# Kernel optimization log

Hardware: AMD Instinct MI355X
Metric: run time of the kernel (lower is better)

## Reference

```python
import jax, jax.numpy as jnp
import numpy as np
import math

NUM_EXPERTS = 8
CAP_FACTOR = 1.25
MIN_CAPACITY = 4

def _capacity(num_tokens, num_experts):
    cap = math.floor(CAP_FACTOR * num_tokens / num_experts)
    cap += cap % 2
    return max(cap, MIN_CAPACITY)

def setup_inputs() -> dict:
    key = jax.random.key(0)
    k1, k2, k3, k4 = jax.random.split(key, 4)
    tokens, d_model, d_ff, E = 8192, 1024, 4096, NUM_EXPERTS
    x = jax.random.normal(k1, (tokens, d_model), dtype=jnp.float32)
    gate_weight = jax.random.normal(k2, (E, d_model), dtype=jnp.float32) * math.sqrt(0.1 / d_model)
    expert_weight = jax.random.normal(k3, (E, d_model, d_ff), dtype=jnp.float32) * 0.02
    expert_bias = jax.random.normal(k4, (E, 1, d_ff), dtype=jnp.float32) * 0.02
    return {"x": x, "gate_weight": gate_weight, "expert_weight": expert_weight, "expert_bias": expert_bias}

def reference(x, gate_weight, expert_weight, expert_bias):
    tokens, d_model = x.shape
    E = gate_weight.shape[0]
    capacity = _capacity(tokens, E)
    # FP32 gate (Switch-style)
    gate_logits = jnp.dot(x.astype(jnp.float32), gate_weight.astype(jnp.float32).T)  # [s, E]
    logits = jax.nn.softmax(gate_logits, axis=-1)  # auto_cast_softmax in fp32
    # Top-1 routing, select_policy='first'
    top1_idx = jnp.argmax(gate_logits, axis=-1)  # argmax over raw gate output
    mask = jax.nn.one_hot(top1_idx, E, dtype=jnp.int32)  # [s, E]
    # aux load-balancing loss (training path)
    me = jnp.mean(logits, axis=0)
    ce = jnp.mean(mask.astype(jnp.float32), axis=0)
    l_aux = E * jnp.sum(me * ce)
    # cumsum-based capacity ranking
    ranks = jnp.cumsum(mask, axis=0) - 1  # [s, E]
    mask = mask * (ranks < capacity).astype(jnp.int32)
    ranks_tok = jnp.sum(mask * ranks, axis=-1)  # [s]
    rank_oh = jax.nn.one_hot(ranks_tok, capacity, dtype=logits.dtype)  # [s, c]
    weight = mask.astype(logits.dtype) * logits  # [s, E]
    combine_weights = weight[:, :, None] * rank_oh[:, None, :]  # [s, E, c]
    sec_mask = combine_weights != 0  # bool dispatch mask
    # scatter dispatch: [s,E,c] x [s,d] -> [E,c,d]
    dispatched = jnp.einsum("sec,sd->ecd", sec_mask.astype(x.dtype), x)
    # per-expert front linear: [E,c,d] x [E,d,f] -> [E,c,f]
    out = jnp.einsum("ecd,edf->ecf", dispatched, expert_weight) + expert_bias
    return out, combine_weights, l_aux
```

## Files before the change

kernel.cpp:

```cpp
#include <hip/hip_runtime.h>
#include <hip/hip_bf16.h>

#define TOKENS 8192
#define DM 1024
#define DFF 4096
#define NE 8
#define CAP 1280
#define ECAP (NE*CAP)
#define OUT_ELEMS ((size_t)NE*CAP*DFF)
#define CMB_ELEMS ((size_t)TOKENS*NE*CAP)
#define ZROW TOKENS
#define GBK 32

typedef __attribute__((ext_vector_type(8))) short short8;
typedef __attribute__((ext_vector_type(16))) float f32x16;
typedef __attribute__((ext_vector_type(4))) float f4;

__device__ inline ushort f2bf(float f) {
    __hip_bfloat16 h = __float2bfloat16(f);
    return *reinterpret_cast<ushort*>(&h);
}

__device__ __forceinline__ void gload16(const ushort* g, short* l) {
    __builtin_amdgcn_global_load_lds(
        (const __attribute__((address_space(1))) void*)g,
        (__attribute__((address_space(3))) void*)l, 16, 0, 0);
}

__global__ __launch_bounds__(256) void gate_kernel(const float* __restrict__ x,
        const float* __restrict__ gw, float* __restrict__ probs8, int* __restrict__ top1,
        ushort* __restrict__ xbf) {
    int wave = threadIdx.x >> 6;
    int lane = threadIdx.x & 63;
    int t = blockIdx.x * 4 + wave;
    const float* xrow = x + (size_t)t * DM;
    float4 xv[4];
    #pragma unroll
    for (int j = 0; j < 4; ++j) xv[j] = *(const float4*)(xrow + lane * 4 + j * 256);
    ushort* xbrow = xbf + (size_t)t * DM;
    #pragma unroll
    for (int j = 0; j < 4; ++j) {
        ushort4 o;
        o.x = f2bf(xv[j].x); o.y = f2bf(xv[j].y); o.z = f2bf(xv[j].z); o.w = f2bf(xv[j].w);
        *(ushort4*)(xbrow + lane * 4 + j * 256) = o;
    }
    float logit[8];
    #pragma unroll
    for (int e = 0; e < 8; ++e) {
        const float* g = gw + e * DM;
        float s = 0.f;
        #pragma unroll
        for (int j = 0; j < 4; ++j) {
            float4 gv = *(const float4*)(g + lane * 4 + j * 256);
            s += xv[j].x * gv.x + xv[j].y * gv.y + xv[j].z * gv.z + xv[j].w * gv.w;
        }
        #pragma unroll
        for (int off = 32; off >= 1; off >>= 1) s += __shfl_xor(s, off);
        logit[e] = s;
    }
    if (lane == 0) {
        int bi = 0; float bv = logit[0];
        #pragma unroll
        for (int e = 1; e < 8; ++e) if (logit[e] > bv) { bv = logit[e]; bi = e; }
        float se = 0.f, p[8];
        #pragma unroll
        for (int e = 0; e < 8; ++e) { p[e] = expf(logit[e] - bv); se += p[e]; }
        float inv = 1.f / se;
        #pragma unroll
        for (int e = 0; e < 8; ++e) probs8[t * 8 + e] = p[e] * inv;
        top1[t] = bi;
    }
    if (blockIdx.x == 0) {
        ushort4 z; z.x = z.y = z.z = z.w = 0;
        *(ushort4*)(xbf + (size_t)ZROW * DM + threadIdx.x * 4) = z;
    }
}

__global__ __launch_bounds__(512) void cvtw_rank_kernel(
        const float* __restrict__ w, ushort* __restrict__ wt,
        const int* __restrict__ top1, const float* __restrict__ probs8,
        int* __restrict__ slot_token, int* __restrict__ pos,
        int* __restrict__ cnts, float* __restrict__ laux_out) {
    __shared__ __align__(16) char smem[TOKENS * 4 + 64 * 4 + 8 * 4];
    const int tid = threadIdx.x;
    if (blockIdx.x == 0) {
        int* t1s = (int*)smem;
        float* red = (float*)(smem + TOKENS * 4);
        int* cnt_sh = (int*)(smem + TOKENS * 4 + 64 * 4);
        int w8 = tid >> 6;
        int lane = tid & 63;
        for (int i = tid; i < TOKENS; i += 512) t1s[i] = top1[i];
        for (int i = tid; i < ECAP; i += 512) slot_token[i] = ZROW;
        for (int i = tid; i < TOKENS; i += 512) pos[i] = -1;

        float ps[8];
        #pragma unroll
        for (int e = 0; e < 8; ++e) ps[e] = 0.f;
        for (int t = tid; t < TOKENS; t += 512) {
            float4 a = *(const float4*)(probs8 + t * 8);
            float4 b = *(const float4*)(probs8 + t * 8 + 4);
            ps[0] += a.x; ps[1] += a.y; ps[2] += a.z; ps[3] += a.w;
            ps[4] += b.x; ps[5] += b.y; ps[6] += b.z; ps[7] += b.w;
        }
        #pragma unroll
        for (int e = 0; e < 8; ++e) {
            #pragma unroll
            for (int off = 32; off >= 1; off >>= 1) ps[e] += __shfl_xor(ps[e], off);
        }
        if (lane == 0) {
            #pragma unroll
            for (int e = 0; e < 8; ++e) red[w8 * 8 + e] = ps[e];
        }
        __syncthreads();

        int base = 0;
        for (int t0 = 0; t0 < TOKENS; t0 += 256) {
            #pragma unroll
            for (int q = 0; q < 4; ++q) {
                int t = t0 + q * 64 + lane;
                bool mine = (t1s[t] == w8);
                unsigned long long m = __ballot(mine);
                if (mine) {
                    int r = base + __popcll(m & ((1ull << lane) - 1ull));
                    if (r < CAP) { slot_token[w8 * CAP + r] = t; pos[t] = w8 * CAP + r; }
                }
                base += __popcll(m);
            }
        }
        if (lane == 0) { cnt_sh[w8] = base; cnts[w8] = (base < CAP) ? base : CAP; }
        __syncthreads();
        if (tid == 0) {
            float la = 0.f;
            #pragma unroll
            for (int e = 0; e < 8; ++e) {
                float me = 0.f;
                #pragma unroll
                for (int wv = 0; wv < 8; ++wv) me += red[wv * 8 + e];
                la += (me / (float)TOKENS) * ((float)cnt_sh[e] / (float)TOKENS);
            }
            laux_out[0] = la * (float)NE;
        }
        return;
    }
    float (*tile)[65] = (float(*)[65])smem;
    int b = blockIdx.x - 1;
    int e = b >> 11;
    int rem = b & 2047;
    int n0 = (rem & 63) * 64;
    int k0 = (rem >> 6) * 32;
    const float* we = w + (size_t)e * DM * DFF;
    int c = tid & 63, r0 = tid >> 6;
    #pragma unroll
    for (int i = 0; i < 4; ++i) {
        int r = r0 + i * 8;
        tile[r][c] = we[(size_t)(k0 + r) * DFF + n0 + c];
    }
    __syncthreads();
    ushort* wte = wt + (size_t)e * DFF * DM;
    int kc = tid & 31, nr0 = tid >> 5;
    #pragma unroll
    for (int i = 0; i < 4; ++i) {
        int nr = nr0 + i * 16;
        wte[(size_t)(n0 + nr) * DM + k0 + kc] = f2bf(tile[kc][nr]);
    }
}

__global__ __launch_bounds__(256, 3) void gemm_kernel(
    const ushort* __restrict__ xbf,
    const ushort* __restrict__ wt,
    const float*  __restrict__ bias,
    const int*    __restrict__ slot_token,
    const int*    __restrict__ cnts,
    float* __restrict__ out,
    const int*    __restrict__ pos,
    const float*  __restrict__ probs8,
    float* __restrict__ cmb,
    int do_combine)
{
    const int bid = blockIdx.x;
    const int e   = bid & 7;
    const int rem = bid >> 3;
    const int nt  = rem & 31;
    const int mt  = rem >> 5;
    __shared__ __align__(16) short lds[2][8192];
    const int tid  = threadIdx.x;
    const int lane = tid & 63;
    const int wave = tid >> 6;
    const int wr = wave >> 1;
    const int wc = wave & 1;
    const int ln31 = lane & 31, lh = lane >> 5;
    const int tbeg = bid * 4;
    const bool has_cmb = do_combine && (bid < 2048);

    float* orow = out + ((size_t)(e * CAP + mt * 128)) * DFF + (size_t)nt * 128;

    if (mt * 128 >= cnts[e]) {
        int c4 = tid & 31;
        int r0b = tid >> 5;
        f4 bv4 = *(const f4*)(bias + e * DFF + nt * 128 + c4 * 4);
        for (int r = r0b; r < 128; r += 8)
            __builtin_nontemporal_store(bv4, (f4*)(orow + (size_t)r * DFF + c4 * 4));
    } else {
        const int r0 = tid >> 2;
        const int kg = (tid & 3) ^ ((tid >> 3) & 3);
        const int tokA0 = slot_token[e * CAP + mt * 128 + r0];
        const int tokA1 = slot_token[e * CAP + mt * 128 + 64 + r0];
        const ushort* aptr0 = xbf + (size_t)tokA0 * DM + kg * 8;
        const ushort* aptr1 = xbf + (size_t)tokA1 * DM + kg * 8;
        const ushort* bptr0 = wt + ((size_t)e * DFF + (size_t)nt * 128 + r0) * DM + kg * 8;
        const ushort* bptr1 = bptr0 + (size_t)64 * DM;

        #define STAGE(T) do { \
            short* base_ = &lds[(T) & 1][0]; \
            size_t ko_ = (size_t)(T) * GBK; \
            gload16(aptr0 + ko_, base_ + tid * 8); \
            gload16(aptr1 + ko_, base_ + 2048 + tid * 8); \
            gload16(bptr0 + ko_, base_ + 4096 + tid * 8); \
            gload16(bptr1 + ko_, base_ + 6144 + tid * 8); \
        } while (0)

        int aoff[4], boff[4];
        #pragma unroll
        for (int s = 0; s < 2; ++s) {
            #pragma unroll
            for (int mi = 0; mi < 2; ++mi) {
                int r = wr * 64 + mi * 32 + ln31;
                int c = lh + 2 * s;
                aoff[s * 2 + mi] = (r * 4 + (c ^ ((r >> 1) & 3))) * 8;
            }
            #pragma unroll
            for (int ni = 0; ni < 2; ++ni) {
                int rn = wc * 64 + ni * 32 + ln31;
                int c = lh + 2 * s;
                boff[s * 2 + ni] = 4096 + (rn * 4 + (c ^ ((rn >> 1) & 3))) * 8;
            }
        }

        f32x16 acc[2][2];
        #pragma unroll
        for (int mi = 0; mi < 2; ++mi)
            #pragma unroll
            for (int ni = 0; ni < 2; ++ni)
                acc[mi][ni] = (f32x16)(0.f);

        STAGE(0);
        for (int t = 0; t < 32; ++t) {
            if (t < 31) {
                STAGE(t + 1);
                asm volatile("s_waitcnt vmcnt(4)" ::: "memory");
            } else {
                asm volatile("s_waitcnt vmcnt(0)" ::: "memory");
            }
            __builtin_amdgcn_s_barrier();
            __builtin_amdgcn_sched_barrier(0);

            const short* L = &lds[t & 1][0];
            __builtin_amdgcn_s_setprio(1);
            #pragma unroll
            for (int s = 0; s < 2; ++s) {
                short8 af[2], bfr[2];
                #pragma unroll
                for (int ni = 0; ni < 2; ++ni) bfr[ni] = *(const short8*)(L + boff[s * 2 + ni]);
                #pragma unroll
                for (int mi = 0; mi < 2; ++mi) af[mi] = *(const short8*)(L + aoff[s * 2 + mi]);
                #pragma unroll
                for (int mi = 0; mi < 2; ++mi)
                    #pragma unroll
                    for (int ni = 0; ni < 2; ++ni)
                        acc[mi][ni] = __builtin_amdgcn_mfma_f32_32x32x16_bf16(af[mi], bfr[ni], acc[mi][ni], 0, 0, 0);
            }
            __builtin_amdgcn_s_setprio(0);
            __builtin_amdgcn_sched_barrier(0);
            asm volatile("" ::: "memory");
            __builtin_amdgcn_s_barrier();
            asm volatile("" ::: "memory");
        }
        #undef STAGE

        #pragma unroll
        for (int ni = 0; ni < 2; ++ni) {
            int c = wc * 64 + ni * 32 + ln31;
            float bv = bias[e * DFF + nt * 128 + c];
            #pragma unroll
            for (int mi = 0; mi < 2; ++mi) {
                #pragma unroll
                for (int reg = 0; reg < 16; ++reg) {
                    int r = wr * 64 + mi * 32 + (reg & 3) + 8 * (reg >> 2) + 4 * lh;
                    __builtin_nontemporal_store(acc[mi][ni][reg] + bv,
                        orow + (size_t)r * DFF + c);
                }
            }
        }
    }

    if (has_cmb) {
        for (int i = 0; i < 4; ++i) {
            int tok = tbeg + i;
            int p = pos[tok];
            int ee = (p < 0) ? 0 : (p / CAP);
            float val = probs8[tok * 8 + ee];
            f4* row = (f4*)(cmb + (size_t)tok * ECAP);
            #pragma unroll
            for (int k = 0; k < 10; ++k) {
                int b4 = (tid + k * 256) * 4;
                f4 v;
                v.x = (b4 + 0 == p) ? val : 0.f;
                v.y = (b4 + 1 == p) ? val : 0.f;
                v.z = (b4 + 2 == p) ? val : 0.f;
                v.w = (b4 + 3 == p) ? val : 0.f;
                __builtin_nontemporal_store(v, row + tid + k * 256);
            }
        }
    }
}

__global__ __launch_bounds__(256) void combine_kernel(const int* __restrict__ pos,
        const float* __restrict__ probs8, float* __restrict__ cmb) {
    int tok = blockIdx.x;
    int p = pos[tok];
    int e = p / CAP;
    float val = probs8[tok * 8 + (e < 0 ? 0 : e)];
    f4* row = (f4*)(cmb + (size_t)tok * ECAP);
    #pragma unroll
    for (int k = 0; k < 10; ++k) {
        int c = threadIdx.x + k * 256;
        int b4 = c * 4;
        f4 v;
        v.x = (b4 + 0 == p) ? val : 0.f;
        v.y = (b4 + 1 == p) ? val : 0.f;
        v.z = (b4 + 2 == p) ? val : 0.f;
        v.w = (b4 + 3 == p) ? val : 0.f;
        __builtin_nontemporal_store(v, row + c);
    }
}

extern "C" void kernel_launch(void* const* d_in, const int* in_sizes, int n_in,
                              void* d_out, int out_size, void* d_ws, size_t ws_size,
                              hipStream_t stream) {
    const float* x  = (const float*)d_in[0];
    const float* gw = (const float*)d_in[1];
    const float* ew = (const float*)d_in[2];
    const float* eb = (const float*)d_in[3];

    float* out = (float*)d_out;
    float* cmb = out + OUT_ELEMS;
    float* laux_out = cmb + CMB_ELEMS;

    float* probs8 = (float*)d_ws;
    int* top1 = (int*)(probs8 + TOKENS * 8);
    int* slot_token = top1 + TOKENS;
    int* pos = slot_token + ECAP;
    int* cnts = pos + TOKENS;

    const size_t SMALL = 1 << 20;
    const size_t WT_ELEMS_ = (size_t)NE * DFF * DM;
    const size_t XBF_ELEMS_ = (size_t)(TOKENS + 1) * DM;
    bool big_ws = ws_size >= SMALL + (WT_ELEMS_ + XBF_ELEMS_) * sizeof(ushort);
    ushort* wtbf = big_ws ? (ushort*)((char*)d_ws + SMALL) : (ushort*)cmb;
    ushort* xbf  = wtbf + WT_ELEMS_;

    gate_kernel<<<TOKENS / 4, 256, 0, stream>>>(x, gw, probs8, top1, xbf);
    cvtw_rank_kernel<<<16385, 512, 0, stream>>>(ew, wtbf, top1, probs8,
                                                slot_token, pos, cnts, laux_out);
    if (big_ws) {
        gemm_kernel<<<2560, 256, 0, stream>>>(xbf, wtbf, eb, slot_token, cnts, out,
                                              pos, probs8, cmb, 1);
    } else {
        gemm_kernel<<<2560, 256, 0, stream>>>(xbf, wtbf, eb, slot_token, cnts, out,
                                              pos, probs8, cmb, 0);
        combine_kernel<<<TOKENS, 256, 0, stream>>>(pos, probs8, cmb);
    }
}
```

Before: 202.7 us.

## Enlarge GEMM tile to 256 rows, triple-buffer LDS, move combine zeroing to convert kernel

The expert GEMM now uses 512-thread blocks computing 256x128 tiles, which halves the grid and the reloads of weight tiles. It prefetches two k-steps ahead through a three-stage LDS ring. The dense zero-fill of the combine-weights tensor moves into extra blocks of the weight-convert/rank kernel. The GEMM then only scatters the single nonzero value per token after its tile. The aims are better operand reuse, more latency hiding, and taking the large combine store stream off the GEMM's critical path. The cost is much more LDS per block, which lowers the number of resident blocks, plus a longer convert kernel.

```diff
diff --git a/kernel.cpp b/kernel.cpp
--- a/kernel.cpp
+++ b/kernel.cpp
@@ -11,6 +11,8 @@
 #define CMB_ELEMS ((size_t)TOKENS*NE*CAP)
 #define ZROW TOKENS
 #define GBK 32
+#define NCVT 16384
+#define NZERO 4096
 
 typedef __attribute__((ext_vector_type(8))) short short8;
 typedef __attribute__((ext_vector_type(16))) float f32x16;
@@ -80,7 +82,8 @@
         const float* __restrict__ w, ushort* __restrict__ wt,
         const int* __restrict__ top1, const float* __restrict__ probs8,
         int* __restrict__ slot_token, int* __restrict__ pos,
-        int* __restrict__ cnts, float* __restrict__ laux_out) {
+        int* __restrict__ cnts, float* __restrict__ laux_out,
+        float* __restrict__ cmb, int do_zero) {
     __shared__ __align__(16) char smem[TOKENS * 4 + 64 * 4 + 8 * 4];
     const int tid = threadIdx.x;
     if (blockIdx.x == 0) {
@@ -142,6 +145,16 @@
         }
         return;
     }
+    if (blockIdx.x > NCVT) {
+        if (!do_zero) return;
+        int zb = blockIdx.x - (NCVT + 1);
+        f4 z4; z4.x = z4.y = z4.z = z4.w = 0.f;
+        f4* row = (f4*)(cmb + (size_t)zb * 2 * ECAP);
+        #pragma unroll
+        for (int k = 0; k < 10; ++k)
+            __builtin_nontemporal_store(z4, row + tid + k * 512);
+        return;
+    }
     float (*tile)[65] = (float(*)[65])smem;
     int b = blockIdx.x - 1;
     int e = b >> 11;
@@ -165,7 +178,7 @@
     }
 }
 
-__global__ __launch_bounds__(256, 3) void gemm_kernel(
+__global__ __launch_bounds__(512, 4) void gemm_kernel(
     const ushort* __restrict__ xbf,
     const ushort* __restrict__ wt,
     const float*  __restrict__ bias,
@@ -175,143 +188,135 @@
     const int*    __restrict__ pos,
     const float*  __restrict__ probs8,
     float* __restrict__ cmb,
-    int do_combine)
+    int do_scatter)
 {
     const int bid = blockIdx.x;
     const int e   = bid & 7;
     const int rem = bid >> 3;
     const int nt  = rem & 31;
     const int mt  = rem >> 5;
-    __shared__ __align__(16) short lds[2][8192];
+    __shared__ __align__(16) short lds[3][12288];
     const int tid  = threadIdx.x;
     const int lane = tid & 63;
     const int wave = tid >> 6;
     const int wr = wave >> 1;
     const int wc = wave & 1;
     const int ln31 = lane & 31, lh = lane >> 5;
-    const int tbeg = bid * 4;
-    const bool has_cmb = do_combine && (bid < 2048);
-
-    float* orow = out + ((size_t)(e * CAP + mt * 128)) * DFF + (size_t)nt * 128;
-
-    if (mt * 128 >= cnts[e]) {
+
+    float* orow = out + ((size_t)(e * CAP + mt * 256)) * DFF + (size_t)nt * 128;
+
+    #define SCATTER() do { if (do_scatter && bid < 1024 && tid < 8) { \
+        int tok_ = bid * 8 + tid; \
+        int p_ = pos[tok_]; \
+        if (p_ >= 0) cmb[(size_t)tok_ * ECAP + p_] = probs8[tok_ * 8 + p_ / CAP]; \
+    } } while (0)
+
+    if (mt * 256 >= cnts[e]) {
         int c4 = tid & 31;
         int r0b = tid >> 5;
         f4 bv4 = *(const f4*)(bias + e * DFF + nt * 128 + c4 * 4);
-        for (int r = r0b; r < 128; r += 8)
+        for (int r = r0b; r < 256; r += 16)
             __builtin_nontemporal_store(bv4, (f4*)(orow + (size_t)r * DFF + c4 * 4));
-    } else {
-        const int r0 = tid >> 2;
-        const int kg = (tid & 3) ^ ((tid >> 3) & 3);
-        const int tokA0 = slot_token[e * CAP + mt * 128 + r0];
-        const int tokA1 = slot_token[e * CAP + mt * 128 + 64 + r0];
-        const ushort* aptr0 = xbf + (size_t)tokA0 * DM + kg * 8;
-        const ushort* aptr1 = xbf + (size_t)tokA1 * DM + kg * 8;
-        const ushort* bptr0 = wt + ((size_t)e * DFF + (size_t)nt * 128 + r0) * DM + kg * 8;
-        const ushort* bptr1 = bptr0 + (size_t)64 * DM;
-
-        #define STAGE(T) do { \
-            short* base_ = &lds[(T) & 1][0]; \
-            size_t ko_ = (size_t)(T) * GBK; \
-            gload16(aptr0 + ko_, base_ + tid * 8); \
-            gload16(aptr1 + ko_, base_ + 2048 + tid * 8); \
-            gload16(bptr0 + ko_, base_ + 4096 + tid * 8); \
-            gload16(bptr1 + ko_, base_ + 6144 + tid * 8); \
-        } while (0)
-
-        int aoff[4], boff[4];
+        SCATTER();
+        return;
+    }
+
+    const int r0a = tid >> 2;
+    const int kg = (tid & 3) ^ ((tid >> 3) & 3);
+    const int tokA0 = slot_token[e * CAP + mt * 256 + r0a];
+    const int tokA1 = slot_token[e * CAP + mt * 256 + 128 + r0a];
+    const ushort* aptr0 = xbf + (size_t)tokA0 * DM + kg * 8;
+    const ushort* aptr1 = xbf + (size_t)tokA1 * DM + kg * 8;
+    const ushort* bptr  = wt + ((size_t)e * DFF + (size_t)nt * 128 + r0a) * DM + kg * 8;
+
+    #define STAGE(T, BUF) do { \
+        short* base_ = &lds[BUF][0]; \
+        size_t ko_ = (size_t)(T) * GBK; \
+        gload16(aptr0 + ko_, base_ + tid * 8); \
+        gload16(aptr1 + ko_, base_ + 4096 + tid * 8); \
+        gload16(bptr  + ko_, base_ + 8192 + tid * 8); \
+    } while (0)
+
+    int aoff[4], boff[4];
+    #pragma unroll
+    for (int s = 0; s < 2; ++s) {
+        #pragma unroll
+        for (int mi = 0; mi < 2; ++mi) {
+            int r = wr * 64 + mi * 32 + ln31;
+            int c = lh + 2 * s;
+            aoff[s * 2 + mi] = (r * 4 + (c ^ ((r >> 1) & 3))) * 8;
+        }
+        #pragma unroll
+        for (int ni = 0; ni < 2; ++ni) {
+            int rn = wc * 64 + ni * 32 + ln31;
+            int c = lh + 2 * s;
+            boff[s * 2 + ni] = 8192 + (rn * 4 + (c ^ ((rn >> 1) & 3))) * 8;
+        }
+    }
+
+    f32x16 acc[2][2];
+    #pragma unroll
+    for (int mi = 0; mi < 2; ++mi)
+        #pragma unroll
+        for (int ni = 0; ni < 2; ++ni)
+            acc[mi][ni] = (f32x16)(0.f);
+
+    STAGE(0, 0); STAGE(1, 1);
+    int cur = 0;
+    int nxt2 = 2;
+    for (int t = 0; t < 32; ++t) {
+        if (t < 30) {
+            STAGE(t + 2, nxt2);
+            asm volatile("s_waitcnt vmcnt(6)" ::: "memory");
+        } else if (t == 30) {
+            asm volatile("s_waitcnt vmcnt(3)" ::: "memory");
+        } else {
+            asm volatile("s_waitcnt vmcnt(0)" ::: "memory");
+        }
+        __builtin_amdgcn_s_barrier();
+        __builtin_amdgcn_sched_barrier(0);
+
+        const short* L = &lds[cur][0];
+        __builtin_amdgcn_s_setprio(1);
         #pragma unroll
         for (int s = 0; s < 2; ++s) {
-            #pragma unroll
-            for (int mi = 0; mi < 2; ++mi) {
-                int r = wr * 64 + mi * 32 + ln31;
-                int c = lh + 2 * s;
-                aoff[s * 2 + mi] = (r * 4 + (c ^ ((r >> 1) & 3))) * 8;
+            short8 af[2], bfr[2];
+            #pragma unroll
+            for (int ni = 0; ni < 2; ++ni) bfr[ni] = *(const short8*)(L + boff[s * 2 + ni]);
+            #pragma unroll
+            for (int mi = 0; mi < 2; ++mi) af[mi] = *(const short8*)(L + aoff[s * 2 + mi]);
+            #pragma unroll
+            for (int mi = 0; mi < 2; ++mi)
+                #pragma unroll
+                for (int ni = 0; ni < 2; ++ni)
+                    acc[mi][ni] = __builtin_amdgcn_mfma_f32_32x32x16_bf16(af[mi], bfr[ni], acc[mi][ni], 0, 0, 0);
+        }
+        __builtin_amdgcn_s_setprio(0);
+        __builtin_amdgcn_sched_barrier(0);
+        asm volatile("" ::: "memory");
+        __builtin_amdgcn_s_barrier();
+        asm volatile("" ::: "memory");
+        cur = (cur == 2) ? 0 : cur + 1;
+        nxt2 = (nxt2 == 2) ? 0 : nxt2 + 1;
+    }
+    #undef STAGE
+
+    #pragma unroll
+    for (int ni = 0; ni < 2; ++ni) {
+        int c = wc * 64 + ni * 32 + ln31;
+        float bv = bias[e * DFF + nt * 128 + c];
+        #pragma unroll
+        for (int mi = 0; mi < 2; ++mi) {
+            #pragma unroll
+            for (int reg = 0; reg < 16; ++reg) {
+                int r = wr * 64 + mi * 32 + (reg & 3) + 8 * (reg >> 2) + 4 * lh;
+                __builtin_nontemporal_store(acc[mi][ni][reg] + bv,
+                    orow + (size_t)r * DFF + c);
             }
-            #pragma unroll
-            for (int ni = 0; ni < 2; ++ni) {
-                int rn = wc * 64 + ni * 32 + ln31;
-                int c = lh + 2 * s;
-                boff[s * 2 + ni] = 4096 + (rn * 4 + (c ^ ((rn >> 1) & 3))) * 8;
-            }
-        }
-
-        f32x16 acc[2][2];
-        #pragma unroll
-        for (int mi = 0; mi < 2; ++mi)
-            #pragma unroll
-            for (int ni = 0; ni < 2; ++ni)
-                acc[mi][ni] = (f32x16)(0.f);
-
-        STAGE(0);
-        for (int t = 0; t < 32; ++t) {
-            if (t < 31) {
-                STAGE(t + 1);
-                asm volatile("s_waitcnt vmcnt(4)" ::: "memory");
-            } else {
-                asm volatile("s_waitcnt vmcnt(0)" ::: "memory");
-            }
-            __builtin_amdgcn_s_barrier();
-            __builtin_amdgcn_sched_barrier(0);
-
-            const short* L = &lds[t & 1][0];
-            __builtin_amdgcn_s_setprio(1);
-            #pragma unroll
-            for (int s = 0; s < 2; ++s) {
-                short8 af[2], bfr[2];
-                #pragma unroll
-                for (int ni = 0; ni < 2; ++ni) bfr[ni] = *(const short8*)(L + boff[s * 2 + ni]);
-                #pragma unroll
-                for (int mi = 0; mi < 2; ++mi) af[mi] = *(const short8*)(L + aoff[s * 2 + mi]);
-                #pragma unroll
-                for (int mi = 0; mi < 2; ++mi)
-                    #pragma unroll
-                    for (int ni = 0; ni < 2; ++ni)
-                        acc[mi][ni] = __builtin_amdgcn_mfma_f32_32x32x16_bf16(af[mi], bfr[ni], acc[mi][ni], 0, 0, 0);
-            }
-            __builtin_amdgcn_s_setprio(0);
-            __builtin_amdgcn_sched_barrier(0);
-            asm volatile("" ::: "memory");
-            __builtin_amdgcn_s_barrier();
-            asm volatile("" ::: "memory");
-        }
-        #undef STAGE
-
-        #pragma unroll
-        for (int ni = 0; ni < 2; ++ni) {
-            int c = wc * 64 + ni * 32 + ln31;
-            float bv = bias[e * DFF + nt * 128 + c];
-            #pragma unroll
-            for (int mi = 0; mi < 2; ++mi) {
-                #pragma unroll
-                for (int reg = 0; reg < 16; ++reg) {
-                    int r = wr * 64 + mi * 32 + (reg & 3) + 8 * (reg >> 2) + 4 * lh;
-                    __builtin_nontemporal_store(acc[mi][ni][reg] + bv,
-                        orow + (size_t)r * DFF + c);
-                }
-            }
-        }
-    }
-
-    if (has_cmb) {
-        for (int i = 0; i < 4; ++i) {
-            int tok = tbeg + i;
-            int p = pos[tok];
-            int ee = (p < 0) ? 0 : (p / CAP);
-            float val = probs8[tok * 8 + ee];
-            f4* row = (f4*)(cmb + (size_t)tok * ECAP);
-            #pragma unroll
-            for (int k = 0; k < 10; ++k) {
-                int b4 = (tid + k * 256) * 4;
-                f4 v;
-                v.x = (b4 + 0 == p) ? val : 0.f;
-                v.y = (b4 + 1 == p) ? val : 0.f;
-                v.z = (b4 + 2 == p) ? val : 0.f;
-                v.w = (b4 + 3 == p) ? val : 0.f;
-                __builtin_nontemporal_store(v, row + tid + k * 256);
-            }
-        }
-    }
+        }
+    }
+    SCATTER();
+    #undef SCATTER
 }
 
 __global__ __launch_bounds__(256) void combine_kernel(const int* __restrict__ pos,
@@ -360,13 +365,13 @@
     ushort* xbf  = wtbf + WT_ELEMS_;
 
     gate_kernel<<<TOKENS / 4, 256, 0, stream>>>(x, gw, probs8, top1, xbf);
-    cvtw_rank_kernel<<<16385, 512, 0, stream>>>(ew, wtbf, top1, probs8,
-                                                slot_token, pos, cnts, laux_out);
+    cvtw_rank_kernel<<<1 + NCVT + NZERO, 512, 0, stream>>>(ew, wtbf, top1, probs8,
+            slot_token, pos, cnts, laux_out, cmb, big_ws ? 1 : 0);
     if (big_ws) {
-        gemm_kernel<<<2560, 256, 0, stream>>>(xbf, wtbf, eb, slot_token, cnts, out,
+        gemm_kernel<<<1280, 512, 0, stream>>>(xbf, wtbf, eb, slot_token, cnts, out,
                                               pos, probs8, cmb, 1);
     } else {
-        gemm_kernel<<<2560, 256, 0, stream>>>(xbf, wtbf, eb, slot_token, cnts, out,
+        gemm_kernel<<<1280, 512, 0, stream>>>(xbf, wtbf, eb, slot_token, cnts, out,
                                               pos, probs8, cmb, 0);
         combine_kernel<<<TOKENS, 256, 0, stream>>>(pos, probs8, cmb);
     }
```

After: 216.6 us. 1.07x slower.
